# Kernel tuning notes

Measured on AMD Instinct MI355X. Metric: run time of the kernel, lower is better.

## Reference

```python
import jax, jax.numpy as jnp
import numpy as np

D_MODEL = 1024
N_HEADS = 16
D_K = D_MODEL // N_HEADS
B, T = 4, 2048


def setup_inputs() -> dict:
    key = jax.random.key(0)
    ks = jax.random.split(key, 12)
    s = 1.0 / np.sqrt(D_MODEL)
    inp = {
        "query": jax.random.normal(ks[0], (B, T, D_MODEL), dtype=jnp.float32),
        "key": jax.random.normal(ks[1], (B, T, D_MODEL), dtype=jnp.float32),
        "value": jax.random.normal(ks[2], (B, T, D_MODEL), dtype=jnp.float32),
        # causal mask, broadcastable over batch and heads
        "mask": jnp.tril(jnp.ones((T, T), dtype=bool))[None, None, :, :],
        "W_q": jax.random.uniform(ks[3], (D_MODEL, D_MODEL), jnp.float32, -s, s),
        "b_q": jnp.zeros((D_MODEL,), jnp.float32),
        "W_k": jax.random.uniform(ks[4], (D_MODEL, D_MODEL), jnp.float32, -s, s),
        "b_k": jnp.zeros((D_MODEL,), jnp.float32),
        "W_v": jax.random.uniform(ks[5], (D_MODEL, D_MODEL), jnp.float32, -s, s),
        "b_v": jnp.zeros((D_MODEL,), jnp.float32),
        "W_o": jax.random.uniform(ks[6], (D_MODEL, D_MODEL), jnp.float32, -s, s),
        "b_o": jnp.zeros((D_MODEL,), jnp.float32),
    }
    return inp


def _split_heads(x):
    b, t, _ = x.shape
    return x.reshape(b, t, N_HEADS, D_K).transpose(0, 2, 1, 3)  # [B,H,T,Dk]


def reference(query, key, value, mask, W_q, b_q, W_k, b_k, W_v, b_v, W_o, b_o):
    q = _split_heads(query @ W_q.T + b_q)
    k = _split_heads(key @ W_k.T + b_k)
    v = _split_heads(value @ W_v.T + b_v)
    scale = 1.0 / jnp.sqrt(jnp.asarray(D_K, q.dtype))
    scores = jnp.einsum("bhqd,bhkd->bhqk", q, k) * scale  # [B,H,Tq,Tk]
    scores = jnp.where(mask, scores, jnp.asarray(-jnp.inf, scores.dtype))
    attn = jax.nn.softmax(scores, axis=-1)
    out = jnp.einsum("bhqk,bhkd->bhqd", attn, v)
    out = out.transpose(0, 2, 1, 3).reshape(query.shape[0], query.shape[1], D_MODEL)
    return out @ W_o.T + b_o
```

## Files before the change

kernel.cpp:

```cpp
#include <hip/hip_runtime.h>
#include <stdint.h>
#include <stddef.h>


typedef __attribute__((ext_vector_type(4))) float f32x4;
typedef __attribute__((ext_vector_type(8))) _Float16 f16x8;
typedef __attribute__((ext_vector_type(4))) _Float16 f16x4;

#define DEV __device__ __forceinline__

constexpr int BATCH = 4, SEQ = 2048, NH = 16, DK = 64, DM = 1024;
constexpr int MROWS = BATCH * SEQ;
constexpr float QSCALE = 0.125f * 1.4426950408889634f;

DEV void async16(const void* g, void* l) {
  __builtin_amdgcn_global_load_lds(
      (const __attribute__((address_space(1))) unsigned int*)g,
      (__attribute__((address_space(3))) unsigned int*)l, 16, 0, 0);
}

__global__ void cvt_w_kernel(const float* __restrict__ w0, const float* __restrict__ w1,
                             const float* __restrict__ w2, const float* __restrict__ w3,
                             _Float16* __restrict__ o0, _Float16* __restrict__ o1,
                             _Float16* __restrict__ o2, _Float16* __restrict__ o3) {
  size_t i = (size_t)blockIdx.x * blockDim.x + threadIdx.x;
  const float* ws[4] = {w0, w1, w2, w3};
  _Float16* os[4] = {o0, o1, o2, o3};
#pragma unroll
  for (int m = 0; m < 4; m++) {
    f32x4 x = *(const f32x4*)(ws[m] + i * 4);
    f16x4 h;
#pragma unroll
    for (int j = 0; j < 4; j++) h[j] = (_Float16)x[j];
    *(f16x4*)(os[m] + i * 4) = h;
  }
}

__global__ void cvt_act_kernel(const float* __restrict__ a0, const float* __restrict__ a1,
                               const float* __restrict__ a2, _Float16* __restrict__ o0,
                               _Float16* __restrict__ o1, _Float16* __restrict__ o2) {
  size_t i = (size_t)blockIdx.x * blockDim.x + threadIdx.x;
  const float* as[3] = {a0, a1, a2};
  _Float16* os[3] = {o0, o1, o2};
#pragma unroll
  for (int m = 0; m < 3; m++) {
    f32x4 x = *(const f32x4*)(as[m] + i * 4);
    f16x4 h;
#pragma unroll
    for (int j = 0; j < 4; j++) h[j] = (_Float16)x[j];
    *(f16x4*)(os[m] + i * 4) = h;
  }
}

struct QKVPtrs {
  const float* a32[3];
  const _Float16* a16[3];
  const _Float16* w[3];
  const float* bias[3];
  _Float16* out[3];
};

template <bool AH>
__global__ __launch_bounds__(256) void gemm_qkv_kernel(QKVPtrs P) {
  constexpr int K = DM;
  __shared__ __align__(16) _Float16 smem[128 * 144];
  _Float16* As = smem;
  _Float16* Bs = smem + 8192;
  const int z = blockIdx.z;
  const _Float16* Bw = P.w[z];
  const int tid = threadIdx.x;
  const int wave = tid >> 6, lane = tid & 63;
  const int quad = lane >> 4, l16 = lane & 15;
  const int wm = wave >> 1, wn = wave & 1;
  const int m0 = blockIdx.x * 128, n0 = blockIdx.y * 128;
  const float scale = (z == 0) ? QSCALE : 1.0f;

  const f32x4 zero4 = {0.f, 0.f, 0.f, 0.f};
  f32x4 acc[4][4];
#pragma unroll
  for (int mt = 0; mt < 4; mt++)
#pragma unroll
    for (int nt = 0; nt < 4; nt++) acc[mt][nt] = zero4;

  float bv[4];
#pragma unroll
  for (int nt = 0; nt < 4; nt++) bv[nt] = P.bias[z][n0 + wn * 64 + nt * 16 + l16];

  for (int kt = 0; kt < K / 64; kt++) {
    const int k0 = kt * 64;
#pragma unroll
    for (int it = 0; it < 4; it++) {
      int idx = it * 256 + tid;
      async16(Bw + (size_t)(n0 + (idx >> 3)) * K + k0 + (idx & 7) * 8,
              (char*)Bs + (size_t)(it * 256 + wave * 64) * 16);
    }
    if (AH) {
      const _Float16* Af = P.a16[z];
#pragma unroll
      for (int it = 0; it < 4; it++) {
        int idx = it * 256 + tid;
        async16(Af + (size_t)(m0 + (idx >> 3)) * K + k0 + (idx & 7) * 8,
                (char*)As + (size_t)(it * 256 + wave * 64) * 16);
      }
    } else {
      const float* Af = P.a32[z];
#pragma unroll
      for (int it = 0; it < 4; it++) {
        int idx = it * 256 + tid;
        int row = idx >> 3, seg = idx & 7;
        const float* g = Af + (size_t)(m0 + row) * K + k0 + seg * 8;
        f32x4 x0 = *(const f32x4*)g;
        f32x4 x1 = *(const f32x4*)(g + 4);
        f16x8 h;
#pragma unroll
        for (int j = 0; j < 4; j++) { h[j] = (_Float16)x0[j]; h[4 + j] = (_Float16)x1[j]; }
        *(f16x8*)&As[row * 64 + seg * 8] = h;
      }
    }
    __syncthreads();
#pragma unroll
    for (int ks = 0; ks < 2; ks++) {
      f16x8 af[4], bfr[4];
#pragma unroll
      for (int mt = 0; mt < 4; mt++)
        af[mt] = *(const f16x8*)&As[(wm * 64 + mt * 16 + l16) * 64 + ks * 32 + quad * 8];
#pragma unroll
      for (int nt = 0; nt < 4; nt++)
        bfr[nt] = *(const f16x8*)&Bs[(wn * 64 + nt * 16 + l16) * 64 + ks * 32 + quad * 8];
#pragma unroll
      for (int mt = 0; mt < 4; mt++)
#pragma unroll
        for (int nt = 0; nt < 4; nt++)
          acc[mt][nt] = __builtin_amdgcn_mfma_f32_16x16x32_f16(af[mt], bfr[nt], acc[mt][nt], 0, 0, 0);
    }
    __syncthreads();
  }

  _Float16* Ct = smem;
  const int b = m0 >> 11, tbase = m0 & (SEQ - 1);
  if (z < 2) {
#pragma unroll
    for (int mt = 0; mt < 4; mt++)
#pragma unroll
      for (int nt = 0; nt < 4; nt++)
#pragma unroll
        for (int i = 0; i < 4; i++)
          Ct[(wm * 64 + mt * 16 + quad * 4 + i) * 144 + wn * 64 + nt * 16 + l16] =
              (_Float16)((acc[mt][nt][i] + bv[nt]) * scale);
  } else {
#pragma unroll
    for (int mt = 0; mt < 4; mt++)
#pragma unroll
      for (int nt = 0; nt < 4; nt++)
#pragma unroll
        for (int i = 0; i < 4; i++)
          Ct[(wn * 64 + nt * 16 + l16) * 144 + wm * 64 + mt * 16 + quad * 4 + i] =
              (_Float16)(acc[mt][nt][i] + bv[nt]);
  }
  __syncthreads();
  _Float16* out = P.out[z];
  if (z < 2) {
    const int row = tid >> 1, coff = (tid & 1) * 32;
#pragma unroll
    for (int hh = 0; hh < 2; hh++) {
      int h = (n0 >> 6) + hh;
      size_t gb = ((size_t)(b * NH + h) * SEQ + tbase) * 64 + (size_t)tid * 32;
#pragma unroll
      for (int k2 = 0; k2 < 4; k2++)
        *(f16x8*)&out[gb + k2 * 8] =
            *(const f16x8*)&Ct[row * 144 + hh * 64 + coff + k2 * 8];
    }
  } else {
#pragma unroll
    for (int k2 = 0; k2 < 8; k2++) {
      int c = k2 * 256 + tid;
      int n = c >> 4, s2 = c & 15;
      int h = (n0 + n) >> 6, d = (n0 + n) & (DK - 1);
      size_t gb = ((size_t)(b * NH + h) * DK + d) * SEQ + tbase + s2 * 8;
      *(f16x8*)&out[gb] = *(const f16x8*)&Ct[n * 144 + s2 * 8];
    }
  }
}

__global__ __launch_bounds__(256) void gemm_out_kernel(
    const _Float16* __restrict__ Ah, const _Float16* __restrict__ Bw,
    const float* __restrict__ bias, float* __restrict__ Cp) {
  constexpr int K = DM;
  __shared__ __align__(16) _Float16 As[128 * 64];
  __shared__ __align__(16) _Float16 Bs[128 * 64];
  const int tid = threadIdx.x;
  const int wave = tid >> 6, lane = tid & 63;
  const int quad = lane >> 4, l16 = lane & 15;
  const int wm = wave >> 1, wn = wave & 1;
  const int m0 = blockIdx.x * 128, n0 = blockIdx.y * 128;

  const f32x4 zero4 = {0.f, 0.f, 0.f, 0.f};
  f32x4 acc[4][4];
#pragma unroll
  for (int mt = 0; mt < 4; mt++)
#pragma unroll
    for (int nt = 0; nt < 4; nt++) acc[mt][nt] = zero4;

  float bv[4];
#pragma unroll
  for (int nt = 0; nt < 4; nt++) bv[nt] = bias[n0 + wn * 64 + nt * 16 + l16];

  for (int kt = 0; kt < K / 64; kt++) {
    const int k0 = kt * 64;
#pragma unroll
    for (int it = 0; it < 4; it++) {
      int idx = it * 256 + tid;
      async16(Bw + (size_t)(n0 + (idx >> 3)) * K + k0 + (idx & 7) * 8,
              (char*)Bs + (size_t)(it * 256 + wave * 64) * 16);
    }
#pragma unroll
    for (int it = 0; it < 4; it++) {
      int idx = it * 256 + tid;
      async16(Ah + (size_t)(m0 + (idx >> 3)) * K + k0 + (idx & 7) * 8,
              (char*)As + (size_t)(it * 256 + wave * 64) * 16);
    }
    __syncthreads();
#pragma unroll
    for (int ks = 0; ks < 2; ks++) {
      f16x8 af[4], bfr[4];
#pragma unroll
      for (int mt = 0; mt < 4; mt++)
        af[mt] = *(const f16x8*)&As[(wm * 64 + mt * 16 + l16) * 64 + ks * 32 + quad * 8];
#pragma unroll
      for (int nt = 0; nt < 4; nt++)
        bfr[nt] = *(const f16x8*)&Bs[(wn * 64 + nt * 16 + l16) * 64 + ks * 32 + quad * 8];
#pragma unroll
      for (int mt = 0; mt < 4; mt++)
#pragma unroll
        for (int nt = 0; nt < 4; nt++)
          acc[mt][nt] = __builtin_amdgcn_mfma_f32_16x16x32_f16(af[mt], bfr[nt], acc[mt][nt], 0, 0, 0);
    }
    __syncthreads();
  }
#pragma unroll
  for (int mt = 0; mt < 4; mt++)
#pragma unroll
    for (int nt = 0; nt < 4; nt++)
#pragma unroll
      for (int i = 0; i < 4; i++) {
        int m = m0 + wm * 64 + mt * 16 + quad * 4 + i;
        int n = n0 + wn * 64 + nt * 16 + l16;
        Cp[(size_t)m * DM + n] = acc[mt][nt][i] + bv[nt];
      }
}

__global__ __launch_bounds__(256, 2) void attn_kernel(
    const _Float16* __restrict__ Q, const _Float16* __restrict__ Kt,
    const _Float16* __restrict__ V, _Float16* __restrict__ O) {
  __shared__ __align__(16) _Float16 Ks[128 * 72];
  __shared__ __align__(16) _Float16 Vs[64 * 136];
  const int tid = threadIdx.x;
  const int wave = tid >> 6, lane = tid & 63, quad = lane >> 4, l16 = lane & 15;
  const int bh = blockIdx.y;
  const size_t base = (size_t)bh * SEQ * DK;
  const int b = bh >> 4, h = bh & 15;
  const f32x4 zero4 = {0.f, 0.f, 0.f, 0.f};

  for (int p = 0; p < 2; p++) {
    const int qt = (p == 0) ? (int)blockIdx.x : 15 - (int)blockIdx.x;
    const int t0 = qt * 128;

    f16x8 qf[2][2];
#pragma unroll
    for (int mt = 0; mt < 2; mt++)
#pragma unroll
      for (int ks = 0; ks < 2; ks++)
        qf[mt][ks] = *(const f16x8*)(Q + base + (size_t)(t0 + wave * 32 + mt * 16 + l16) * DK +
                                     ks * 32 + quad * 8);

    f32x4 oacc[2][4];
#pragma unroll
    for (int mt = 0; mt < 2; mt++)
#pragma unroll
      for (int nt = 0; nt < 4; nt++) oacc[mt][nt] = zero4;
    float mrow[2] = {-1e30f, -1e30f}, lrow[2] = {0.f, 0.f};

    for (int j = 0; j <= qt; j++) {
#pragma unroll
      for (int it = 0; it < 4; it++) {
        int c = it * 256 + tid;
        int row = c >> 3, off = (c & 7) * 8;
        *(f16x8*)&Ks[row * 72 + off] =
            *(const f16x8*)(Kt + base + (size_t)(j * 128 + row) * 64 + off);
      }
#pragma unroll
      for (int it = 0; it < 4; it++) {
        int c = it * 256 + tid;
        int d = c >> 4, off = (c & 15) * 8;
        *(f16x8*)&Vs[d * 136 + off] =
            *(const f16x8*)(V + base + ((size_t)d << 11) + j * 128 + off);
      }
      __syncthreads();

      f32x4 s[2][8];
#pragma unroll
      for (int nt = 0; nt < 8; nt++) {
        f16x8 kf0 = *(const f16x8*)&Ks[(nt * 16 + l16) * 72 + quad * 8];
        f16x8 kf1 = *(const f16x8*)&Ks[(nt * 16 + l16) * 72 + 32 + quad * 8];
#pragma unroll
        for (int mt = 0; mt < 2; mt++) {
          f32x4 zz = zero4;
          zz = __builtin_amdgcn_mfma_f32_16x16x32_f16(kf0, qf[mt][0], zz, 0, 0, 0);
          zz = __builtin_amdgcn_mfma_f32_16x16x32_f16(kf1, qf[mt][1], zz, 0, 0, 0);
          s[mt][nt] = zz;
        }
      }
      if (j == qt) {
#pragma unroll
        for (int mt = 0; mt < 2; mt++) {
          int qloc = wave * 32 + mt * 16 + l16;
#pragma unroll
          for (int nt = 0; nt < 8; nt++)
#pragma unroll
            for (int i = 0; i < 4; i++)
              if (nt * 16 + quad * 4 + i > qloc) s[mt][nt][i] = -1e30f;
        }
      }
#pragma unroll
      for (int mt = 0; mt < 2; mt++) {
        float mx = mrow[mt];
#pragma unroll
        for (int nt = 0; nt < 8; nt++)
#pragma unroll
          for (int i = 0; i < 4; i++) mx = fmaxf(mx, s[mt][nt][i]);
        mx = fmaxf(mx, __shfl_xor(mx, 16));
        mx = fmaxf(mx, __shfl_xor(mx, 32));
        float alpha = __builtin_exp2f(mrow[mt] - mx);
        mrow[mt] = mx;
        float rs = 0.f;
#pragma unroll
        for (int nt = 0; nt < 8; nt++)
#pragma unroll
          for (int i = 0; i < 4; i++) {
            float pv = __builtin_exp2f(s[mt][nt][i] - mx);
            s[mt][nt][i] = pv;
            rs += pv;
          }
        rs += __shfl_xor(rs, 16);
        rs += __shfl_xor(rs, 32);
        lrow[mt] = lrow[mt] * alpha + rs;
#pragma unroll
        for (int i = 0; i < 4; i++) {
          float ab = __shfl(alpha, quad * 4 + i);
#pragma unroll
          for (int nt = 0; nt < 4; nt++) oacc[mt][nt][i] *= ab;
        }
      }
#pragma unroll
      for (int jj = 0; jj < 8; jj++) {
        f16x4 pf[2];
#pragma unroll
        for (int mt = 0; mt < 2; mt++) {
          f16x4 t;
#pragma unroll
          for (int i = 0; i < 4; i++) t[i] = (_Float16)s[mt][jj][i];
          pf[mt] = t;
        }
#pragma unroll
        for (int nt = 0; nt < 4; nt++) {
          f16x4 vb = *(const f16x4*)&Vs[(nt * 16 + l16) * 136 + jj * 16 + quad * 4];
#pragma unroll
          for (int mt = 0; mt < 2; mt++)
            oacc[mt][nt] = __builtin_amdgcn_mfma_f32_16x16x16f16(pf[mt], vb, oacc[mt][nt], 0, 0, 0);
        }
      }
      __syncthreads();
    }
#pragma unroll
    for (int mt = 0; mt < 2; mt++) {
      float linv = 1.0f / lrow[mt];
#pragma unroll
      for (int i = 0; i < 4; i++) {
        float lb = __shfl(linv, quad * 4 + i);
        int t = t0 + wave * 32 + mt * 16 + quad * 4 + i;
#pragma unroll
        for (int nt = 0; nt < 4; nt++) {
          int d = nt * 16 + l16;
          O[((size_t)(b * SEQ + t) << 10) + h * 64 + d] = (_Float16)(oacc[mt][nt][i] * lb);
        }
      }
    }
  }
}

extern "C" void kernel_launch(void* const* d_in, const int* in_sizes, int n_in,
                              void* d_out, int out_size, void* d_ws, size_t ws_size,
                              hipStream_t stream) {
  const float* query = (const float*)d_in[0];
  const float* key_  = (const float*)d_in[1];
  const float* value = (const float*)d_in[2];
  const float* W_q = (const float*)d_in[4];
  const float* b_q = (const float*)d_in[5];
  const float* W_k = (const float*)d_in[6];
  const float* b_k = (const float*)d_in[7];
  const float* W_v = (const float*)d_in[8];
  const float* b_v = (const float*)d_in[9];
  const float* W_o = (const float*)d_in[10];
  const float* b_o = (const float*)d_in[11];

  constexpr size_t WEL = (size_t)DM * DM;
  constexpr size_t MEL = (size_t)MROWS * DM;
  _Float16* ws = (_Float16*)d_ws;
  _Float16* wq = ws;
  _Float16* wk = wq + WEL;
  _Float16* wv = wk + WEL;
  _Float16* wo = wv + WEL;

  const bool big = ws_size >= (size_t)(4 * WEL + 6 * MEL) * sizeof(_Float16);

  QKVPtrs P;
  P.a32[0] = query; P.a32[1] = key_; P.a32[2] = value;
  P.w[0] = wq; P.w[1] = wk; P.w[2] = wv;
  P.bias[0] = b_q; P.bias[1] = b_k; P.bias[2] = b_v;

  cvt_w_kernel<<<dim3((unsigned)(WEL / 4 / 256)), 256, 0, stream>>>(
      W_q, W_k, W_v, W_o, wq, wk, wv, wo);

  _Float16 *qb, *kb, *vb, *ab;
  if (big) {
    _Float16* qh = wo + WEL;
    _Float16* kh = qh + MEL;
    _Float16* vh = kh + MEL;
    qb = vh + MEL; kb = qb + MEL; vb = kb + MEL;
    ab = qh;
    P.a16[0] = qh; P.a16[1] = kh; P.a16[2] = vh;
    P.out[0] = qb; P.out[1] = kb; P.out[2] = vb;
    cvt_act_kernel<<<dim3((unsigned)(MEL / 4 / 256)), 256, 0, stream>>>(
        query, key_, value, qh, kh, vh);
    gemm_qkv_kernel<true><<<dim3(MROWS / 128, DM / 128, 3), 256, 0, stream>>>(P);
  } else {
    qb = wo + WEL; kb = qb + MEL; vb = kb + MEL; ab = vb + MEL;
    P.a16[0] = P.a16[1] = P.a16[2] = nullptr;
    P.out[0] = qb; P.out[1] = kb; P.out[2] = vb;
    gemm_qkv_kernel<false><<<dim3(MROWS / 128, DM / 128, 3), 256, 0, stream>>>(P);
  }

  attn_kernel<<<dim3(8, BATCH * NH), 256, 0, stream>>>(qb, kb, vb, ab);

  gemm_out_kernel<<<dim3(MROWS / 128, DM / 128), 256, 0, stream>>>(ab, wo, b_o, (float*)d_out);
}
```

Measured before the change: 366.1 us.

## Double-buffer GEMM LDS tiles with XOR swizzle and MFMA priority

Both projection GEMMs (QKV and output) now keep two LDS buffers, so loading the next K-tile overlaps MFMA work on the current one. This removes one barrier per iteration. Tiles are stored with an XOR swizzle on the 16-byte segment index to cut LDS bank conflicts on the fragment reads, and s_setprio raises wave priority during the MFMA phase. LDS use doubles to 64KB per block, which may lower occupancy. The fp32 A path still does synchronous loads and converts, so it gets less overlap.

```diff
diff --git a/kernel.cpp b/kernel.cpp
--- a/kernel.cpp
+++ b/kernel.cpp
@@ -60,12 +60,36 @@
   _Float16* out[3];
 };
 
+DEV void stage_g16(const _Float16* __restrict__ src, int k0, _Float16* dst, int tid) {
+  const int wave = tid >> 6;
+#pragma unroll
+  for (int it = 0; it < 4; it++) {
+    int idx = it * 256 + tid;
+    int row = idx >> 3, seg = idx & 7;
+    async16(src + (size_t)row * DM + k0 + ((seg ^ (row & 7)) << 3),
+            (char*)dst + (size_t)(it * 256 + wave * 64) * 16);
+  }
+}
+
+DEV void stage_f32(const float* __restrict__ src, int k0, _Float16* dst, int tid) {
+#pragma unroll
+  for (int it = 0; it < 4; it++) {
+    int idx = it * 256 + tid;
+    int row = idx >> 3, seg = idx & 7;
+    const float* g = src + (size_t)row * DM + k0 + seg * 8;
+    f32x4 x0 = *(const f32x4*)g;
+    f32x4 x1 = *(const f32x4*)(g + 4);
+    f16x8 h;
+#pragma unroll
+    for (int j = 0; j < 4; j++) { h[j] = (_Float16)x0[j]; h[4 + j] = (_Float16)x1[j]; }
+    *(f16x8*)&dst[row * 64 + ((seg ^ (row & 7)) << 3)] = h;
+  }
+}
+
 template <bool AH>
 __global__ __launch_bounds__(256) void gemm_qkv_kernel(QKVPtrs P) {
   constexpr int K = DM;
-  __shared__ __align__(16) _Float16 smem[128 * 144];
-  _Float16* As = smem;
-  _Float16* Bs = smem + 8192;
+  __shared__ __align__(16) _Float16 smem[4 * 128 * 64];
   const int z = blockIdx.z;
   const _Float16* Bw = P.w[z];
   const int tid = threadIdx.x;
@@ -75,6 +99,10 @@
   const int m0 = blockIdx.x * 128, n0 = blockIdx.y * 128;
   const float scale = (z == 0) ? QSCALE : 1.0f;
 
+  const _Float16* Bg = Bw + (size_t)n0 * K;
+  const _Float16* Ag16 = AH ? P.a16[z] + (size_t)m0 * K : nullptr;
+  const float* Ag32 = AH ? nullptr : P.a32[z] + (size_t)m0 * K;
+
   const f32x4 zero4 = {0.f, 0.f, 0.f, 0.f};
   f32x4 acc[4][4];
 #pragma unroll
@@ -86,53 +114,43 @@
 #pragma unroll
   for (int nt = 0; nt < 4; nt++) bv[nt] = P.bias[z][n0 + wn * 64 + nt * 16 + l16];
 
+  stage_g16(Bg, 0, smem + 8192, tid);
+  if (AH) stage_g16(Ag16, 0, smem, tid);
+  else    stage_f32(Ag32, 0, smem, tid);
+  __syncthreads();
+
   for (int kt = 0; kt < K / 64; kt++) {
-    const int k0 = kt * 64;
-#pragma unroll
-    for (int it = 0; it < 4; it++) {
-      int idx = it * 256 + tid;
-      async16(Bw + (size_t)(n0 + (idx >> 3)) * K + k0 + (idx & 7) * 8,
-              (char*)Bs + (size_t)(it * 256 + wave * 64) * 16);
-    }
-    if (AH) {
-      const _Float16* Af = P.a16[z];
-#pragma unroll
-      for (int it = 0; it < 4; it++) {
-        int idx = it * 256 + tid;
-        async16(Af + (size_t)(m0 + (idx >> 3)) * K + k0 + (idx & 7) * 8,
-                (char*)As + (size_t)(it * 256 + wave * 64) * 16);
-      }
-    } else {
-      const float* Af = P.a32[z];
-#pragma unroll
-      for (int it = 0; it < 4; it++) {
-        int idx = it * 256 + tid;
-        int row = idx >> 3, seg = idx & 7;
-        const float* g = Af + (size_t)(m0 + row) * K + k0 + seg * 8;
-        f32x4 x0 = *(const f32x4*)g;
-        f32x4 x1 = *(const f32x4*)(g + 4);
-        f16x8 h;
-#pragma unroll
-        for (int j = 0; j < 4; j++) { h[j] = (_Float16)x0[j]; h[4 + j] = (_Float16)x1[j]; }
-        *(f16x8*)&As[row * 64 + seg * 8] = h;
-      }
-    }
-    __syncthreads();
+    const int boff = (kt & 1) ? 16384 : 0;
+    const _Float16* Asc = smem + boff;
+    const _Float16* Bsc = smem + 8192 + boff;
+    if (kt + 1 < K / 64) {
+      const int k0 = (kt + 1) * 64;
+      const int poff = boff ^ 16384;
+      stage_g16(Bg, k0, smem + 8192 + poff, tid);
+      if (AH) stage_g16(Ag16, k0, smem + poff, tid);
+      else    stage_f32(Ag32, k0, smem + poff, tid);
+    }
+    __builtin_amdgcn_s_setprio(1);
 #pragma unroll
     for (int ks = 0; ks < 2; ks++) {
       f16x8 af[4], bfr[4];
 #pragma unroll
-      for (int mt = 0; mt < 4; mt++)
-        af[mt] = *(const f16x8*)&As[(wm * 64 + mt * 16 + l16) * 64 + ks * 32 + quad * 8];
-#pragma unroll
-      for (int nt = 0; nt < 4; nt++)
-        bfr[nt] = *(const f16x8*)&Bs[(wn * 64 + nt * 16 + l16) * 64 + ks * 32 + quad * 8];
+      for (int mt = 0; mt < 4; mt++) {
+        int r = wm * 64 + mt * 16 + l16;
+        af[mt] = *(const f16x8*)&Asc[r * 64 + (((ks * 4 + quad) ^ (r & 7)) << 3)];
+      }
+#pragma unroll
+      for (int nt = 0; nt < 4; nt++) {
+        int r = wn * 64 + nt * 16 + l16;
+        bfr[nt] = *(const f16x8*)&Bsc[r * 64 + (((ks * 4 + quad) ^ (r & 7)) << 3)];
+      }
 #pragma unroll
       for (int mt = 0; mt < 4; mt++)
 #pragma unroll
         for (int nt = 0; nt < 4; nt++)
           acc[mt][nt] = __builtin_amdgcn_mfma_f32_16x16x32_f16(af[mt], bfr[nt], acc[mt][nt], 0, 0, 0);
     }
+    __builtin_amdgcn_s_setprio(0);
     __syncthreads();
   }
 
@@ -186,14 +204,16 @@
     const _Float16* __restrict__ Ah, const _Float16* __restrict__ Bw,
     const float* __restrict__ bias, float* __restrict__ Cp) {
   constexpr int K = DM;
-  __shared__ __align__(16) _Float16 As[128 * 64];
-  __shared__ __align__(16) _Float16 Bs[128 * 64];
+  __shared__ __align__(16) _Float16 smem[4 * 128 * 64];
   const int tid = threadIdx.x;
   const int wave = tid >> 6, lane = tid & 63;
   const int quad = lane >> 4, l16 = lane & 15;
   const int wm = wave >> 1, wn = wave & 1;
   const int m0 = blockIdx.x * 128, n0 = blockIdx.y * 128;
 
+  const _Float16* Bg = Bw + (size_t)n0 * K;
+  const _Float16* Ag = Ah + (size_t)m0 * K;
+
   const f32x4 zero4 = {0.f, 0.f, 0.f, 0.f};
   f32x4 acc[4][4];
 #pragma unroll
@@ -205,36 +225,41 @@
 #pragma unroll
   for (int nt = 0; nt < 4; nt++) bv[nt] = bias[n0 + wn * 64 + nt * 16 + l16];
 
+  stage_g16(Bg, 0, smem + 8192, tid);
+  stage_g16(Ag, 0, smem, tid);
+  __syncthreads();
+
   for (int kt = 0; kt < K / 64; kt++) {
-    const int k0 = kt * 64;
-#pragma unroll
-    for (int it = 0; it < 4; it++) {
-      int idx = it * 256 + tid;
-      async16(Bw + (size_t)(n0 + (idx >> 3)) * K + k0 + (idx & 7) * 8,
-              (char*)Bs + (size_t)(it * 256 + wave * 64) * 16);
-    }
-#pragma unroll
-    for (int it = 0; it < 4; it++) {
-      int idx = it * 256 + tid;
-      async16(Ah + (size_t)(m0 + (idx >> 3)) * K + k0 + (idx & 7) * 8,
-              (char*)As + (size_t)(it * 256 + wave * 64) * 16);
-    }
-    __syncthreads();
+    const int boff = (kt & 1) ? 16384 : 0;
+    const _Float16* Asc = smem + boff;
+    const _Float16* Bsc = smem + 8192 + boff;
+    if (kt + 1 < K / 64) {
+      const int k0 = (kt + 1) * 64;
+      const int poff = boff ^ 16384;
+      stage_g16(Bg, k0, smem + 8192 + poff, tid);
+      stage_g16(Ag, k0, smem + poff, tid);
+    }
+    __builtin_amdgcn_s_setprio(1);
 #pragma unroll
     for (int ks = 0; ks < 2; ks++) {
       f16x8 af[4], bfr[4];
 #pragma unroll
-      for (int mt = 0; mt < 4; mt++)
-        af[mt] = *(const f16x8*)&As[(wm * 64 + mt * 16 + l16) * 64 + ks * 32 + quad * 8];
-#pragma unroll
-      for (int nt = 0; nt < 4; nt++)
-        bfr[nt] = *(const f16x8*)&Bs[(wn * 64 + nt * 16 + l16) * 64 + ks * 32 + quad * 8];
+      for (int mt = 0; mt < 4; mt++) {
+        int r = wm * 64 + mt * 16 + l16;
+        af[mt] = *(const f16x8*)&Asc[r * 64 + (((ks * 4 + quad) ^ (r & 7)) << 3)];
+      }
+#pragma unroll
+      for (int nt = 0; nt < 4; nt++) {
+        int r = wn * 64 + nt * 16 + l16;
+        bfr[nt] = *(const f16x8*)&Bsc[r * 64 + (((ks * 4 + quad) ^ (r & 7)) << 3)];
+      }
 #pragma unroll
       for (int mt = 0; mt < 4; mt++)
 #pragma unroll
         for (int nt = 0; nt < 4; nt++)
           acc[mt][nt] = __builtin_amdgcn_mfma_f32_16x16x32_f16(af[mt], bfr[nt], acc[mt][nt], 0, 0, 0);
     }
+    __builtin_amdgcn_s_setprio(0);
     __syncthreads();
   }
 #pragma unroll
```

Result: faster. 329.7 us (-9.9%).
